# Performance work log

Measured on AMD Instinct MI355X. Metric: run time of the kernel, lower is better.

The kernel has to match this reference:

```python
import jax, jax.numpy as jnp
import numpy as np

N_NODE = 118
DM, DP, DR, DH, DN, DPHI, DE = 768, 128, 128, 256, 256, 192, 256
N_OUT = 2
NEG = -1e9

leaky = lambda z: jnp.where(z >= 0, z, 0.01 * z)


def lstm_layer(x_seq, W_ih, W_hh, b_ih, b_hh):
    # x_seq: [B, T, in]; W_ih: [4H, in]; W_hh: [4H, H]; gate order i,f,g,o (torch)
    B = x_seq.shape[0]
    H = W_hh.shape[1]

    def step(carry, xt):
        h, c = carry
        gates = xt @ W_ih.T + h @ W_hh.T + b_ih + b_hh  # [B, 4H]
        i, f, g, o = jnp.split(gates, 4, axis=1)
        c = jax.nn.sigmoid(f) * c + jax.nn.sigmoid(i) * jnp.tanh(g)
        h = jax.nn.sigmoid(o) * jnp.tanh(c)
        return (h, c), h

    h0 = jnp.zeros((B, H), x_seq.dtype)
    (_, _), hs = jax.lax.scan(step, (h0, h0), jnp.swapaxes(x_seq, 0, 1))
    return jnp.swapaxes(hs, 0, 1)  # [B, T, H]


def setup_inputs() -> dict:
    key = jax.random.key(0)
    ks = jax.random.split(key, 32)
    n_feat, T = 128, 2048
    sc = 0.05
    inp = {}
    inp["x"] = jax.random.normal(ks[0], (N_NODE, T, n_feat), jnp.float32)
    h_pmt = jax.random.uniform(ks[1], (N_NODE, 2), jnp.float32)
    act = jax.random.randint(ks[2], (N_NODE, 1), 0, 2).astype(jnp.float32)
    inp["x_tag"] = jnp.concatenate([h_pmt, act], axis=1)
    # LSTM params (2 layers, hidden=DP)
    inp["W_ih0"] = jax.random.normal(ks[3], (4 * DP, n_feat), jnp.float32) * sc
    inp["W_hh0"] = jax.random.normal(ks[4], (4 * DP, DP), jnp.float32) * sc
    inp["b_ih0"] = jnp.zeros((4 * DP,), jnp.float32)
    inp["b_hh0"] = jnp.zeros((4 * DP,), jnp.float32)
    inp["W_ih1"] = jax.random.normal(ks[5], (4 * DP, DP), jnp.float32) * sc
    inp["W_hh1"] = jax.random.normal(ks[6], (4 * DP, DP), jnp.float32) * sc
    inp["b_ih1"] = jnp.zeros((4 * DP,), jnp.float32)
    inp["b_hh1"] = jnp.zeros((4 * DP,), jnp.float32)
    inp["pseudo_message"] = jax.random.normal(ks[7], (1, DM), jnp.float32) * sc
    inp["Wum"] = jax.random.normal(ks[8], (DM + 1, DR), jnp.float32) * sc
    inp["Wvm"] = jax.random.normal(ks[9], (DM + 1, DR), jnp.float32) * sc
    inp["Wup"] = jax.random.normal(ks[10], (DP, DR), jnp.float32) * sc
    inp["Wvp"] = jax.random.normal(ks[11], (DP, DR), jnp.float32) * sc
    inp["W_hyb"] = jax.random.normal(ks[12], (3 * DR, DH), jnp.float32) * sc
    inp["b_hyb"] = jnp.zeros((DH,), jnp.float32)
    inp["W_act"] = jax.random.normal(ks[13], (DH + 2, DN), jnp.float32) * sc
    inp["b_act"] = jnp.zeros((DN,), jnp.float32)
    inp["W_inact"] = jax.random.normal(ks[14], (DH, DN), jnp.float32) * sc
    inp["b_inact"] = jnp.zeros((DN,), jnp.float32)
    inp["Wphin"] = jax.random.normal(ks[15], (2 * DN, DPHI), jnp.float32) * sc
    inp["aphi"] = jax.random.normal(ks[16], (DPHI, 1), jnp.float32) * sc
    inp["Won"] = jax.random.normal(ks[17], (2 * DN, DN), jnp.float32) * sc
    inp["Weo"] = jax.random.normal(ks[18], (3 * DN, DE), jnp.float32) * sc
    inp["Wi"] = jax.random.normal(ks[19], (N_NODE, DN + 2 * DE, N_OUT), jnp.float32) * sc
    inp["bi"] = jax.random.normal(ks[20], (N_NODE, N_OUT), jnp.float32) * sc
    return inp


def reference(x, x_tag, W_ih0, W_hh0, b_ih0, b_hh0, W_ih1, W_hh1, b_ih1, b_hh1,
              pseudo_message, Wum, Wvm, Wup, Wvp, W_hyb, b_hyb, W_act, b_act,
              W_inact, b_inact, Wphin, aphi, Won, Weo, Wi, bi):
    N = x.shape[0]
    # --- price embedding: 2-layer LSTM, take last hidden ---
    h1 = lstm_layer(x, W_ih0, W_hh0, b_ih0, b_hh0)
    h2 = lstm_layer(h1, W_ih1, W_hh1, b_ih1, b_hh1)
    p = leaky(h2[:, -1, :])  # [N, DP]

    act = x_tag[:, -1:]                      # [N, 1]
    V1 = x_tag[:, -1] == 0
    V0 = x_tag[:, -1] == 1
    m = jnp.broadcast_to(pseudo_message, (N, DM))
    v_m = leaky(jnp.concatenate([m, act], axis=1) @ Wvm)
    u_p = leaky(p @ Wup)
    h_pmt = x_tag[:, 0:2]
    h_hyb = leaky(jnp.concatenate([u_p, u_p + v_m, v_m], axis=1) @ W_hyb + b_hyb)
    n_act = (jnp.concatenate([h_hyb, h_pmt], axis=1) @ W_act + b_act) * (1.0 - act)
    n_inact = (h_hyb @ W_inact + b_inact) * act
    n = leaky(n_act + n_inact)               # [N, DN]

    # pair[i, j] = cat(n[j], n[i])  (matches unsqueeze(0)/unsqueeze(1) repeat order)
    pair = jnp.concatenate([
        jnp.broadcast_to(n[None, :, :], (N, N, DN)),
        jnp.broadcast_to(n[:, None, :], (N, N, DN)),
    ], axis=-1)                               # [N, N, 2*DN]

    phi = (leaky(pair @ Wphin) @ aphi)[..., 0]  # [N, N]
    mask1 = V1[:, None]
    mask0 = V0[:, None]
    phi1 = jax.nn.softmax(jnp.where(mask1, phi, NEG), axis=0)
    phi0 = jax.nn.softmax(jnp.where(mask0, phi, NEG), axis=0)
    phi_masked = jnp.where(mask1, phi1, jnp.where(mask0, phi0, phi))
    phi_all = jax.nn.softmax(phi, axis=0)
    alpha = jnp.where(jnp.sum(V1) > 0, phi_masked, phi_all)

    e = leaky(pair @ Won)
    e = jnp.concatenate([e, pair], axis=-1) @ Weo  # [N, N, DE]
    alpha1 = (1.0 - act) * alpha              # [N, N]
    alpha0 = act * alpha
    hyper_m1 = leaky(jnp.einsum('nj,njd->nd', alpha1, e))
    hyper_m0 = leaky(jnp.einsum('nj,njd->nd', alpha0, e))
    hyper_m = jnp.concatenate([hyper_m0, hyper_m1], axis=-1)
    output = jnp.concatenate([n, hyper_m], axis=-1)  # [N, DN+2*DE]
    y_hat = jnp.einsum('nd,ndo->no', output, Wi) + bi
    y_hat = jax.nn.softmax(y_hat, axis=1)

    o1 = Wum @ Wvm.T
    o2 = Wup @ Wvp.T
    l_ort = jnp.sqrt(jnp.sum(o1 * o1)) + jnp.sqrt(jnp.sum(o2 * o2))

    # vectorized pairwise cosine similarity * sign product over V1 nodes
    nrm = jnp.maximum(jnp.linalg.norm(n, axis=1), 1e-8)
    n_unit = n / nrm[:, None]
    s = jnp.sign(h_pmt[:, 1] - h_pmt[:, 0]) * V1.astype(n.dtype)
    l_pol = jnp.sum((n_unit @ n_unit.T) * (s[:, None] * s[None, :]))

    return (y_hat, h_pmt, l_ort, l_pol, V1, V0)
```

## Files before the change

kernel.cpp:

```cpp
#include <hip/hip_runtime.h>
#include <cstdint>
#include <cstddef>

#define NNODE 118
#define TSEQ  2048
#define TC    256
#define NCH   8
#define TGB   8
#define NEGC  -1000000000.0f

typedef __fp16 f16x8 __attribute__((ext_vector_type(8)));
typedef float floatx4 __attribute__((ext_vector_type(4)));

__device__ __forceinline__ float leakyf(float x){ return x >= 0.f ? x : 0.01f * x; }
__device__ __forceinline__ float frcp(float x){ return __builtin_amdgcn_rcpf(x); }
__device__ __forceinline__ float sigm(float x){ return frcp(1.f + __expf(-x)); }
__device__ __forceinline__ float tanhfast(float x){ return 1.f - 2.f * frcp(__expf(2.f * x) + 1.f); }

__device__ __forceinline__ int swzb(int row, int colByte){
  return row * 256 + (colByte ^ ((row & 7) << 4) ^ ((row & 8) << 2));
}

__device__ float bred_sum(float v, float* buf, int nthr){
  int tid = threadIdx.x;
  buf[tid] = v; __syncthreads();
  for (int s = nthr >> 1; s > 0; s >>= 1){
    if (tid < s) buf[tid] += buf[tid + s];
    __syncthreads();
  }
  float r = buf[0]; __syncthreads(); return r;
}
__device__ float bred_max(float v, float* buf, int nthr){
  int tid = threadIdx.x;
  buf[tid] = v; __syncthreads();
  for (int s = nthr >> 1; s > 0; s >>= 1){
    if (tid < s) buf[tid] = fmaxf(buf[tid], buf[tid + s]);
    __syncthreads();
  }
  float r = buf[0]; __syncthreads(); return r;
}

__global__ void f32_to_f16_k(const float* __restrict__ in, __fp16* __restrict__ out, int n){
  int i = blockIdx.x * blockDim.x + threadIdx.x;
  if (i < n) out[i] = (__fp16)in[i];
}

__global__ __launch_bounds__(256, 2) void gateproj(
    const float* __restrict__ x,
    const __fp16* __restrict__ ringr,
    const __fp16* __restrict__ wiA,
    const __fp16* __restrict__ wiB,
    __fp16* __restrict__ pre1o, __fp16* __restrict__ pre2o,
    int n1blocks, int t0abs)
{
  const int tid = threadIdx.x, lane = tid & 63, w4 = tid >> 6;
  const int q = lane >> 4, l16 = lane & 15;
  const bool isA = (int)blockIdx.x < n1blocks;
  const int bid = isA ? blockIdx.x : (blockIdx.x - n1blocks);
  const int tg = bid >> 3, blk = bid & 7, tbase = tg * TGB;
  const __fp16* Wf = isA ? wiA : wiB;
  __fp16* preo = isA ? pre1o : pre2o;

  __shared__ __fp16 tiles[TGB][2048];

  if (isA){
    const int node = tid >> 4, k8 = tid & 15;
    const int gnode = blk * 16 + node;
    #pragma unroll
    for (int t = 0; t < TGB; t++){
      __fp16 tmp[8];
      if (gnode < NNODE){
        const float* s = x + ((size_t)gnode * TSEQ + (t0abs + tbase + t)) * 128 + k8 * 8;
        float4 a = ((const float4*)s)[0];
        float4 b = ((const float4*)s)[1];
        tmp[0]=(__fp16)a.x; tmp[1]=(__fp16)a.y; tmp[2]=(__fp16)a.z; tmp[3]=(__fp16)a.w;
        tmp[4]=(__fp16)b.x; tmp[5]=(__fp16)b.y; tmp[6]=(__fp16)b.z; tmp[7]=(__fp16)b.w;
      } else {
        #pragma unroll
        for (int i = 0; i < 8; i++) tmp[i] = (__fp16)0.f;
      }
      *(uint4*)((char*)&tiles[t][0] + swzb(node, k8 * 16)) = *(const uint4*)tmp;
    }
  } else {
    #pragma unroll
    for (int t = 0; t < TGB; t++){
      uint4 v = *(const uint4*)((const char*)ringr + (((size_t)(tbase + t) * 8 + blk) * 4096) + tid * 16);
      *(uint4*)((char*)&tiles[t][0] + tid * 16) = v;
    }
  }

  f16x8 WB[2][4][4];
  #pragma unroll
  for (int ws = 0; ws < 2; ws++)
    #pragma unroll
    for (int g = 0; g < 4; g++){
      const int gate = g * 128 + (w4 * 2 + ws) * 16 + l16;
      const __fp16* wp = Wf + (size_t)gate * 128 + q * 8;
      #pragma unroll
      for (int kt = 0; kt < 4; kt++) WB[ws][g][kt] = *(const f16x8*)(wp + kt * 32);
    }
  __syncthreads();

  #pragma unroll 1
  for (int t = 0; t < TGB; t++){
    f16x8 ax[4];
    #pragma unroll
    for (int kt = 0; kt < 4; kt++)
      ax[kt] = *(const f16x8*)((const char*)&tiles[t][0] + swzb(l16, kt * 64 + q * 16));
    #pragma unroll
    for (int ws = 0; ws < 2; ws++){
      const size_t off = ((((size_t)(tbase + t) * 8 + blk) * 8 + (size_t)(w4 * 2 + ws)) * 64 + (size_t)lane) * 32;
      #pragma unroll
      for (int g = 0; g < 4; g++){
        floatx4 acc = {0.f, 0.f, 0.f, 0.f};
        #pragma unroll
        for (int kt = 0; kt < 4; kt++)
          acc = __builtin_amdgcn_mfma_f32_16x16x32_f16(ax[kt], WB[ws][g][kt], acc, 0, 0, 0);
        __fp16 o[4];
        o[0]=(__fp16)acc[0]; o[1]=(__fp16)acc[1]; o[2]=(__fp16)acc[2]; o[3]=(__fp16)acc[3];
        *(uint2*)((char*)preo + off + g * 8) = *(const uint2*)o;
      }
    }
  }
}

__global__ __launch_bounds__(512, 2) void lstm_scan(
    const __fp16* __restrict__ pre1, const __fp16* __restrict__ pre2,
    __fp16* __restrict__ ring,
    const __fp16* __restrict__ whh0, const __fp16* __restrict__ whh1,
    const float* __restrict__ b_ih0, const float* __restrict__ b_hh0,
    const float* __restrict__ b_ih1, const float* __restrict__ b_hh1,
    __fp16* __restrict__ hs1, float* __restrict__ c1s,
    __fp16* __restrict__ hs2, float* __restrict__ c2s,
    float* __restrict__ pout, int c)
{
  const bool isL1 = blockIdx.x < 8;
  if (isL1){ if (c >= NCH) return; } else { if (c < 1) return; }
  const int blk = blockIdx.x & 7, n0 = blk * 16;
  const int tid = threadIdx.x, lane = tid & 63, w = tid >> 6;
  const int q = lane >> 4, l16 = lane & 15;

  __shared__ __fp16 hhist[16][2048];

  const __fp16* prebase = isL1 ? pre1 : pre2;
  const __fp16* Wh = isL1 ? whh0 : whh1;
  const float* bA = isL1 ? b_ih0 : b_ih1;
  const float* bB = isL1 ? b_hh0 : b_hh1;
  __fp16* hst = isL1 ? hs1 : hs2;
  float* cst = isL1 ? c1s : c2s;
  const bool zin = isL1 ? (c == 0) : (c == 1);
  char* ringw = (char*)(ring + (size_t)(c & 1) * TC * 8 * 2048);

  f16x8 WH[4][4];
  float bias[4];
  #pragma unroll
  for (int g = 0; g < 4; g++){
    const int gate = g * 128 + w * 16 + l16;
    const __fp16* wp = Wh + (size_t)gate * 128 + q * 8;
    #pragma unroll
    for (int kt = 0; kt < 4; kt++) WH[g][kt] = *(const f16x8*)(wp + kt * 32);
    bias[g] = bA[gate] + bB[gate];
  }

  float creg[4]; __fp16 hreg[4];
  #pragma unroll
  for (int r = 0; r < 4; r++){
    const int node = q * 4 + r, d = w * 16 + l16;
    __fp16 h0;
    if (zin){ creg[r] = 0.f; h0 = (__fp16)0.f; }
    else { creg[r] = cst[(size_t)(n0 + node) * 128 + d]; h0 = hst[(size_t)(n0 + node) * 128 + d]; }
    hreg[r] = h0;
    *(__fp16*)((char*)&hhist[15][0] + swzb(node, 2 * d)) = h0;
  }

#define LDPRE(PR, T) do { \
    const char* _b = (const char*)prebase + ((((size_t)(T) * 8 + blk) * 8 + (size_t)w) * 64 + (size_t)lane) * 32; \
    PR[0] = ((const uint4*)_b)[0]; \
    PR[1] = ((const uint4*)_b)[1]; \
  } while (0)

#define STEP(P, CUR, NXT) do { \
    const char* hsrc = (const char*)&hhist[((P) + 15) & 15][0]; \
    if (isL1 && (P) >= 8 && (((P) & 7) == 0)){ \
      const int half_ = ((P) & 8) ? 0 : 8;       \
      _Pragma("unroll") \
      for (int s_ = 0; s_ < 8; s_++){ \
        uint2 hv = *(const uint2*)((const char*)&hhist[half_ + s_][0] + tid * 8); \
        *(uint2*)(ringw + (((size_t)((P) - 8 + s_) * 8 + blk) * 4096) + tid * 8) = hv; \
      } \
    } \
    floatx4 acc[4]; \
    { \
      __fp16 pva[8], pvb[8]; \
      *(uint4*)pva = CUR[0]; *(uint4*)pvb = CUR[1]; \
      _Pragma("unroll") \
      for (int i_ = 0; i_ < 4; i_++){ \
        acc[0][i_] = (float)pva[i_];     acc[1][i_] = (float)pva[4 + i_]; \
        acc[2][i_] = (float)pvb[i_];     acc[3][i_] = (float)pvb[4 + i_]; \
      } \
    } \
    if ((P) + 1 < TC) LDPRE(NXT, (P) + 1); \
    f16x8 ah[4]; \
    _Pragma("unroll") \
    for (int kt = 0; kt < 4; kt++) \
      ah[kt] = *(const f16x8*)(hsrc + swzb(l16, kt * 64 + q * 16)); \
    _Pragma("unroll") \
    for (int kt = 0; kt < 4; kt++){ \
      _Pragma("unroll") \
      for (int g = 0; g < 4; g++) \
        acc[g] = __builtin_amdgcn_mfma_f32_16x16x32_f16(ah[kt], WH[g][kt], acc[g], 0, 0, 0); \
    } \
    char* hdst = (char*)&hhist[(P) & 15][0]; \
    _Pragma("unroll") \
    for (int r = 0; r < 4; r++){ \
      const float gi = acc[0][r] + bias[0]; \
      const float gf = acc[1][r] + bias[1]; \
      const float gc = acc[2][r] + bias[2]; \
      const float go = acc[3][r] + bias[3]; \
      float cc = sigm(gf) * creg[r] + sigm(gi) * tanhfast(gc); \
      creg[r] = cc; \
      const float h = sigm(go) * tanhfast(cc); \
      hreg[r] = (__fp16)h; \
      *(__fp16*)(hdst + swzb(q * 4 + r, 2 * (w * 16 + l16))) = hreg[r]; \
    } \
    __syncthreads(); \
  } while (0)

  uint4 prA[2], prB[2];
  LDPRE(prA, 0);
  __syncthreads();

  #pragma unroll 1
  for (int p = 0; p < TC; p += 2){
    STEP(p, prA, prB);
    STEP(p + 1, prB, prA);
  }

  if (isL1){
    #pragma unroll
    for (int s_ = 0; s_ < 8; s_++){
      uint2 hv = *(const uint2*)((const char*)&hhist[8 + s_][0] + tid * 8);
      *(uint2*)(ringw + (((size_t)(TC - 8 + s_) * 8 + blk) * 4096) + tid * 8) = hv;
    }
  }
  #pragma unroll
  for (int r = 0; r < 4; r++){
    const int node = q * 4 + r, d = w * 16 + l16;
    const size_t idx = (size_t)(n0 + node) * 128 + d;
    cst[idx] = creg[r];
    hst[idx] = hreg[r];
    if (!isL1 && c == NCH && (n0 + node) < NNODE) pout[idx] = leakyf((float)hreg[r]);
  }
#undef STEP
#undef LDPRE
}

__global__ void node_mlp(
    const float* __restrict__ x_tag, const float* __restrict__ pm,
    const float* __restrict__ Wvm, const float* __restrict__ Wup,
    const float* __restrict__ W_hyb, const float* __restrict__ b_hyb,
    const float* __restrict__ W_act, const float* __restrict__ b_act,
    const float* __restrict__ W_inact, const float* __restrict__ b_inact,
    const float* __restrict__ p, float* __restrict__ nmat)
{
  int n = blockIdx.x, tid = threadIdx.x;
  __shared__ float pl[128], up[128], vm[128], hh[256];
  float act = x_tag[n * 3 + 2], hp0 = x_tag[n * 3 + 0], hp1 = x_tag[n * 3 + 1];
  if (tid < 128) pl[tid] = p[n * 128 + tid];
  __syncthreads();
  if (tid < 128){
    float a1 = 0.f;
    for (int k = 0; k < 768; k++) a1 += pm[k] * Wvm[k * 128 + tid];
    a1 += act * Wvm[768 * 128 + tid];
    vm[tid] = leakyf(a1);
    float a2 = 0.f;
    for (int k = 0; k < 128; k++) a2 += pl[k] * Wup[k * 128 + tid];
    up[tid] = leakyf(a2);
  }
  __syncthreads();
  {
    float a = b_hyb[tid];
    for (int k = 0; k < 128; k++) a += up[k] * W_hyb[k * 256 + tid];
    for (int k = 0; k < 128; k++) a += (up[k] + vm[k]) * W_hyb[(128 + k) * 256 + tid];
    for (int k = 0; k < 128; k++) a += vm[k] * W_hyb[(256 + k) * 256 + tid];
    hh[tid] = leakyf(a);
  }
  __syncthreads();
  {
    float na = b_act[tid];
    for (int k = 0; k < 256; k++) na += hh[k] * W_act[k * 256 + tid];
    na += hp0 * W_act[256 * 256 + tid] + hp1 * W_act[257 * 256 + tid];
    float ni = b_inact[tid];
    for (int k = 0; k < 256; k++) ni += hh[k] * W_inact[k * 256 + tid];
    nmat[n * 256 + tid] = leakyf(na * (1.f - act) + ni * act);
  }
}

__global__ void node_proj(
    const float* __restrict__ nmat,
    const float* __restrict__ Wphin, const float* __restrict__ Won,
    const float* __restrict__ Weo,
    float* __restrict__ A, float* __restrict__ B,
    float* __restrict__ C, float* __restrict__ D,
    float* __restrict__ Q, float* __restrict__ R)
{
  int n = blockIdx.x, tid = threadIdx.x;
  __shared__ float nl[256];
  nl[tid] = nmat[n * 256 + tid];
  __syncthreads();
  if (tid < 192){
    float a = 0.f, b = 0.f;
    for (int k = 0; k < 256; k++){ float v = nl[k]; a += v * Wphin[k * 192 + tid]; b += v * Wphin[(256 + k) * 192 + tid]; }
    A[n * 192 + tid] = a; B[n * 192 + tid] = b;
  }
  float c = 0.f, d = 0.f, q = 0.f, r = 0.f;
  for (int k = 0; k < 256; k++){
    float v = nl[k];
    c += v * Won[k * 256 + tid];
    d += v * Won[(256 + k) * 256 + tid];
    q += v * Weo[(256 + k) * 256 + tid];
    r += v * Weo[(512 + k) * 256 + tid];
  }
  C[n * 256 + tid] = c; D[n * 256 + tid] = d;
  Q[n * 256 + tid] = q; R[n * 256 + tid] = r;
}

__global__ void phi_kernel(const float* __restrict__ A, const float* __restrict__ B,
                           const float* __restrict__ aphi, float* __restrict__ phiT)
{
  int j = blockIdx.x, tid = threadIdx.x;
  __shared__ float Aj[192], ap[192];
  for (int k = tid; k < 192; k += 128){ Aj[k] = A[j * 192 + k]; ap[k] = aphi[k]; }
  __syncthreads();
  if (tid < NNODE){
    const float* Bi = B + (size_t)tid * 192;
    float s = 0.f;
    for (int k = 0; k < 192; k++) s += leakyf(Aj[k] + Bi[k]) * ap[k];
    phiT[j * NNODE + tid] = s;
  }
}

__global__ void alpha_kernel(const float* __restrict__ phiT, const float* __restrict__ x_tag,
                             float* __restrict__ alpha)
{
  int j = blockIdx.x, tid = threadIdx.x;
  __shared__ float buf[128];
  bool valid = tid < NNODE;
  float ph = valid ? phiT[j * NNODE + tid] : 0.f;
  float a  = valid ? x_tag[tid * 3 + 2] : -1.f;
  bool v1 = (a == 0.f), v0 = (a == 1.f);

  float c1 = bred_sum((valid && v1) ? 1.f : 0.f, buf, 128);

  float x1 = (valid && v1) ? ph : NEGC;
  float m1 = bred_max(valid ? x1 : -3.4e38f, buf, 128);
  float e1 = valid ? __expf(x1 - m1) : 0.f;
  float s1 = bred_sum(e1, buf, 128);
  float p1 = e1 / s1;

  float x0 = (valid && v0) ? ph : NEGC;
  float m0 = bred_max(valid ? x0 : -3.4e38f, buf, 128);
  float e0 = valid ? __expf(x0 - m0) : 0.f;
  float s0 = bred_sum(e0, buf, 128);
  float p0 = e0 / s0;

  float ma = bred_max(valid ? ph : -3.4e38f, buf, 128);
  float ea = valid ? __expf(ph - ma) : 0.f;
  float sa = bred_sum(ea, buf, 128);
  float pa = ea / sa;

  float pmask = v1 ? p1 : (v0 ? p0 : ph);
  float al = (c1 > 0.f) ? pmask : pa;
  if (valid) alpha[tid * NNODE + j] = al;
}

__global__ void att_sum(const float* __restrict__ alpha, const float* __restrict__ C,
                        const float* __restrict__ D, const float* __restrict__ Q,
                        const float* __restrict__ R, const float* __restrict__ nmat,
                        float* __restrict__ T1, float* __restrict__ Spart,
                        float* __restrict__ nrm)
{
  int i = blockIdx.x, tid = threadIdx.x;
  __shared__ float al[128];
  __shared__ float rb[256];
  if (tid < 128) al[tid] = (tid < NNODE) ? alpha[i * NNODE + tid] : 0.f;
  __syncthreads();
  float Di = D[i * 256 + tid];
  float acc1 = 0.f, acc2 = 0.f, sa = 0.f;
  for (int jj = 0; jj < NNODE; jj++){
    float av = al[jj]; sa += av;
    acc1 += av * leakyf(C[jj * 256 + tid] + Di);
    acc2 += av * Q[jj * 256 + tid];
  }
  T1[i * 256 + tid] = acc1;
  Spart[i * 256 + tid] = acc2 + sa * R[i * 256 + tid];
  float nv = nmat[i * 256 + tid];
  float ss = bred_sum(nv * nv, rb, 256);
  if (tid == 0) nrm[i] = fmaxf(sqrtf(ss), 1e-8f);
}

__global__ void finalize_node(const float* __restrict__ T1, const float* __restrict__ Spart,
                              const float* __restrict__ Weo, const float* __restrict__ nmat,
                              const float* __restrict__ x_tag, const float* __restrict__ Wi,
                              const float* __restrict__ bi, const float* __restrict__ nrm,
                              float* __restrict__ vvec, float* __restrict__ out)
{
  int i = blockIdx.x, tid = threadIdx.x;
  __shared__ float t1[256];
  __shared__ float rb[256];
  t1[tid] = T1[i * 256 + tid];
  __syncthreads();
  float s = Spart[i * 256 + tid];
  for (int k = 0; k < 256; k++) s += t1[k] * Weo[k * 256 + tid];
  float act = x_tag[i * 3 + 2], hp0 = x_tag[i * 3 + 0], hp1 = x_tag[i * 3 + 1];
  float hm0 = leakyf(act * s);
  float hm1 = leakyf((1.f - act) * s);
  float nd = nmat[i * 256 + tid];
  const float* Wir = Wi + (size_t)i * 1536;
  float y0 = nd * Wir[tid * 2]     + hm0 * Wir[(256 + tid) * 2]     + hm1 * Wir[(512 + tid) * 2];
  float y1 = nd * Wir[tid * 2 + 1] + hm0 * Wir[(256 + tid) * 2 + 1] + hm1 * Wir[(512 + tid) * 2 + 1];
  y0 = bred_sum(y0, rb, 256);
  y1 = bred_sum(y1, rb, 256);
  float sgn = (hp1 > hp0) ? 1.f : ((hp1 < hp0) ? -1.f : 0.f);
  if (act == 0.f && sgn != 0.f) atomicAdd(vvec + tid, sgn * nd / nrm[i]);
  if (tid == 0){
    y0 += bi[i * 2]; y1 += bi[i * 2 + 1];
    float m = fmaxf(y0, y1);
    float ee0 = __expf(y0 - m), ee1 = __expf(y1 - m);
    float ssum = ee0 + ee1;
    out[i * 2]     = ee0 / ssum;
    out[i * 2 + 1] = ee1 / ssum;
    out[236 + i * 2]     = hp0;
    out[236 + i * 2 + 1] = hp1;
    out[474 + i] = (act == 0.f) ? 1.f : 0.f;
    out[592 + i] = (act == 1.f) ? 1.f : 0.f;
  }
}

__global__ void ort_kernel(const float* __restrict__ Wum, const float* __restrict__ Wvm,
                           const float* __restrict__ Wup, const float* __restrict__ Wvp,
                           float* __restrict__ misc)
{
  int a = blockIdx.x, b = threadIdx.x;
  float g1 = 0.f, g2 = 0.f, g3 = 0.f, g4 = 0.f;
  for (int r = 0; r < 769; r++){
    g1 += Wum[r * 128 + a] * Wum[r * 128 + b];
    g2 += Wvm[r * 128 + a] * Wvm[r * 128 + b];
  }
  for (int r = 0; r < 128; r++){
    g3 += Wup[r * 128 + a] * Wup[r * 128 + b];
    g4 += Wvp[r * 128 + a] * Wvp[r * 128 + b];
  }
  __shared__ float rb[128];
  float s1 = bred_sum(g1 * g2, rb, 128);
  float s2 = bred_sum(g3 * g4, rb, 128);
  if (b == 0){ atomicAdd(misc + 0, s1); atomicAdd(misc + 1, s2); }
}

__global__ void finalize_scalars(const float* __restrict__ misc, const float* __restrict__ vvec,
                                 float* __restrict__ out)
{
  __shared__ float rb[256];
  int tid = threadIdx.x;
  float v = vvec[tid];
  float ss = bred_sum(v * v, rb, 256);
  if (tid == 0){
    out[472] = sqrtf(misc[0]) + sqrtf(misc[1]);
    out[473] = ss;
  }
}

extern "C" void kernel_launch(void* const* d_in, const int* in_sizes, int n_in,
                              void* d_out, int out_size, void* d_ws, size_t ws_size,
                              hipStream_t stream)
{
  const float* x        = (const float*)d_in[0];
  const float* x_tag    = (const float*)d_in[1];
  const float* W_ih0    = (const float*)d_in[2];
  const float* W_hh0    = (const float*)d_in[3];
  const float* b_ih0    = (const float*)d_in[4];
  const float* b_hh0    = (const float*)d_in[5];
  const float* W_ih1    = (const float*)d_in[6];
  const float* W_hh1    = (const float*)d_in[7];
  const float* b_ih1    = (const float*)d_in[8];
  const float* b_hh1    = (const float*)d_in[9];
  const float* pm       = (const float*)d_in[10];
  const float* Wum      = (const float*)d_in[11];
  const float* Wvm      = (const float*)d_in[12];
  const float* Wup      = (const float*)d_in[13];
  const float* Wvp      = (const float*)d_in[14];
  const float* W_hyb    = (const float*)d_in[15];
  const float* b_hyb    = (const float*)d_in[16];
  const float* W_act    = (const float*)d_in[17];
  const float* b_act    = (const float*)d_in[18];
  const float* W_inact  = (const float*)d_in[19];
  const float* b_inact  = (const float*)d_in[20];
  const float* Wphin    = (const float*)d_in[21];
  const float* aphi     = (const float*)d_in[22];
  const float* Won      = (const float*)d_in[23];
  const float* Weo      = (const float*)d_in[24];
  const float* Wi       = (const float*)d_in[25];
  const float* bi       = (const float*)d_in[26];
  float* out = (float*)d_out;

  char* base = (char*)d_ws;
  size_t off = 0;
  auto take = [&](size_t bytes) -> char* {
    char* p = base + off;
    off += (bytes + 255) & ~(size_t)255;
    return p;
  };
  __fp16* pre1   = (__fp16*)take((size_t)TC * 8 * 32 * 512);
  __fp16* pre2   = (__fp16*)take((size_t)TC * 8 * 32 * 512);
  __fp16* h1ring = (__fp16*)take((size_t)2 * TC * 8 * 2048 * 2);
  __fp16* wih0h  = (__fp16*)take((size_t)512 * 128 * 2);
  __fp16* wih1h  = (__fp16*)take((size_t)512 * 128 * 2);
  __fp16* whh0h  = (__fp16*)take((size_t)512 * 128 * 2);
  __fp16* whh1h  = (__fp16*)take((size_t)512 * 128 * 2);
  __fp16* hs1    = (__fp16*)take((size_t)128 * 128 * 2);
  float* c1s     = (float*)take((size_t)128 * 128 * 4);
  __fp16* hs2    = (__fp16*)take((size_t)128 * 128 * 2);
  float* c2s     = (float*)take((size_t)128 * 128 * 4);
  float* pbuf  = (float*)take((size_t)NNODE * 128 * 4);
  float* nmat  = (float*)take((size_t)NNODE * 256 * 4);
  float* Amat  = (float*)take((size_t)NNODE * 192 * 4);
  float* Bmat  = (float*)take((size_t)NNODE * 192 * 4);
  float* Cmat  = (float*)take((size_t)NNODE * 256 * 4);
  float* Dmat  = (float*)take((size_t)NNODE * 256 * 4);
  float* Qmat  = (float*)take((size_t)NNODE * 256 * 4);
  float* Rmat  = (float*)take((size_t)NNODE * 256 * 4);
  float* phiT  = (float*)take((size_t)NNODE * NNODE * 4);
  float* alpha = (float*)take((size_t)NNODE * NNODE * 4);
  float* T1    = (float*)take((size_t)NNODE * 256 * 4);
  float* Spart = (float*)take((size_t)NNODE * 256 * 4);
  float* nrm   = (float*)take((size_t)NNODE * 4);
  float* vvec  = (float*)take(256 * 4);
  float* misc  = (float*)take(8 * 4);

  hipMemsetAsync(vvec, 0, 1024 + 32, stream);

  f32_to_f16_k<<<256, 256, 0, stream>>>(W_ih0, wih0h, 512 * 128);
  f32_to_f16_k<<<256, 256, 0, stream>>>(W_ih1, wih1h, 512 * 128);
  f32_to_f16_k<<<256, 256, 0, stream>>>(W_hh0, whh0h, 512 * 128);
  f32_to_f16_k<<<256, 256, 0, stream>>>(W_hh1, whh1h, 512 * 128);

  const size_t ringslot = (size_t)TC * 8 * 2048;
  const int gpb = (TC / TGB) * 8;
  for (int c = 0; c <= NCH; c++){
    const int n1 = (c < NCH) ? gpb : 0;
    const int n2 = (c >= 1) ? gpb : 0;
    if (n1 + n2 > 0)
      gateproj<<<n1 + n2, 256, 0, stream>>>(x, h1ring + (size_t)((c - 1) & 1) * ringslot,
                                            wih0h, wih1h, pre1, pre2, n1, c * TC);
    lstm_scan<<<16, 512, 0, stream>>>(pre1, pre2, h1ring, whh0h, whh1h,
                                      b_ih0, b_hh0, b_ih1, b_hh1,
                                      hs1, c1s, hs2, c2s, pbuf, c);
  }

  node_mlp<<<NNODE, 256, 0, stream>>>(x_tag, pm, Wvm, Wup, W_hyb, b_hyb,
                                      W_act, b_act, W_inact, b_inact, pbuf, nmat);
  node_proj<<<NNODE, 256, 0, stream>>>(nmat, Wphin, Won, Weo, Amat, Bmat, Cmat, Dmat, Qmat, Rmat);
  phi_kernel<<<NNODE, 128, 0, stream>>>(Amat, Bmat, aphi, phiT);
  alpha_kernel<<<NNODE, 128, 0, stream>>>(phiT, x_tag, alpha);
  att_sum<<<NNODE, 256, 0, stream>>>(alpha, Cmat, Dmat, Qmat, Rmat, nmat, T1, Spart, nrm);
  finalize_node<<<NNODE, 256, 0, stream>>>(T1, Spart, Weo, nmat, x_tag, Wi, bi, nrm, vvec, out);
  ort_kernel<<<128, 128, 0, stream>>>(Wum, Wvm, Wup, Wvp, misc);
  finalize_scalars<<<1, 256, 0, stream>>>(misc, vvec, out);
}
```

Baseline: 3.350 ms.

## Fold LSTM bias into gate projection, deepen prefetch, and slim scan step barrier

Moves the bias addition out of the sequential LSTM scan into the parallel gate projection kernel, shortening the per-step critical path. The precomputed-gate prefetch now runs two steps ahead instead of one. The LSTM cell math is rewritten to share reciprocals, so one cell update uses two rcp instead of five. __syncthreads is replaced by an explicit LDS waitcnt plus s_barrier, so outstanding global loads are not waited on at each step. Adding bias before the fp16 rounding of the pre-activations slightly changes numerics, and the combined-fraction form could overflow for large gate values.

```diff
diff --git a/kernel.cpp b/kernel.cpp
--- a/kernel.cpp
+++ b/kernel.cpp
@@ -50,6 +50,8 @@
     const __fp16* __restrict__ ringr,
     const __fp16* __restrict__ wiA,
     const __fp16* __restrict__ wiB,
+    const float* __restrict__ bA_ih, const float* __restrict__ bA_hh,
+    const float* __restrict__ bB_ih, const float* __restrict__ bB_hh,
     __fp16* __restrict__ pre1o, __fp16* __restrict__ pre2o,
     int n1blocks, int t0abs)
 {
@@ -59,6 +61,8 @@
   const int bid = isA ? blockIdx.x : (blockIdx.x - n1blocks);
   const int tg = bid >> 3, blk = bid & 7, tbase = tg * TGB;
   const __fp16* Wf = isA ? wiA : wiB;
+  const float* bih = isA ? bA_ih : bB_ih;
+  const float* bhh = isA ? bA_hh : bB_hh;
   __fp16* preo = isA ? pre1o : pre2o;
 
   __shared__ __fp16 tiles[TGB][2048];
@@ -90,6 +94,7 @@
   }
 
   f16x8 WB[2][4][4];
+  float bsum[2][4];
   #pragma unroll
   for (int ws = 0; ws < 2; ws++)
     #pragma unroll
@@ -98,6 +103,7 @@
       const __fp16* wp = Wf + (size_t)gate * 128 + q * 8;
       #pragma unroll
       for (int kt = 0; kt < 4; kt++) WB[ws][g][kt] = *(const f16x8*)(wp + kt * 32);
+      bsum[ws][g] = bih[gate] + bhh[gate];
     }
   __syncthreads();
 
@@ -117,7 +123,9 @@
         for (int kt = 0; kt < 4; kt++)
           acc = __builtin_amdgcn_mfma_f32_16x16x32_f16(ax[kt], WB[ws][g][kt], acc, 0, 0, 0);
         __fp16 o[4];
-        o[0]=(__fp16)acc[0]; o[1]=(__fp16)acc[1]; o[2]=(__fp16)acc[2]; o[3]=(__fp16)acc[3];
+        const float bb = bsum[ws][g];
+        o[0]=(__fp16)(acc[0]+bb); o[1]=(__fp16)(acc[1]+bb);
+        o[2]=(__fp16)(acc[2]+bb); o[3]=(__fp16)(acc[3]+bb);
         *(uint2*)((char*)preo + off + g * 8) = *(const uint2*)o;
       }
     }
@@ -128,8 +136,6 @@
     const __fp16* __restrict__ pre1, const __fp16* __restrict__ pre2,
     __fp16* __restrict__ ring,
     const __fp16* __restrict__ whh0, const __fp16* __restrict__ whh1,
-    const float* __restrict__ b_ih0, const float* __restrict__ b_hh0,
-    const float* __restrict__ b_ih1, const float* __restrict__ b_hh1,
     __fp16* __restrict__ hs1, float* __restrict__ c1s,
     __fp16* __restrict__ hs2, float* __restrict__ c2s,
     float* __restrict__ pout, int c)
@@ -144,22 +150,18 @@
 
   const __fp16* prebase = isL1 ? pre1 : pre2;
   const __fp16* Wh = isL1 ? whh0 : whh1;
-  const float* bA = isL1 ? b_ih0 : b_ih1;
-  const float* bB = isL1 ? b_hh0 : b_hh1;
   __fp16* hst = isL1 ? hs1 : hs2;
   float* cst = isL1 ? c1s : c2s;
   const bool zin = isL1 ? (c == 0) : (c == 1);
   char* ringw = (char*)(ring + (size_t)(c & 1) * TC * 8 * 2048);
 
   f16x8 WH[4][4];
-  float bias[4];
   #pragma unroll
   for (int g = 0; g < 4; g++){
     const int gate = g * 128 + w * 16 + l16;
     const __fp16* wp = Wh + (size_t)gate * 128 + q * 8;
     #pragma unroll
     for (int kt = 0; kt < 4; kt++) WH[g][kt] = *(const f16x8*)(wp + kt * 32);
-    bias[g] = bA[gate] + bB[gate];
   }
 
   float creg[4]; __fp16 hreg[4];
@@ -179,7 +181,14 @@
     PR[1] = ((const uint4*)_b)[1]; \
   } while (0)
 
-#define STEP(P, CUR, NXT) do { \
+#define SYNC() do { \
+    __builtin_amdgcn_sched_barrier(0); \
+    asm volatile("s_waitcnt lgkmcnt(0)"); \
+    __builtin_amdgcn_sched_barrier(0); \
+    __builtin_amdgcn_s_barrier(); \
+  } while (0)
+
+#define STEP(P, CUR) do { \
     const char* hsrc = (const char*)&hhist[((P) + 15) & 15][0]; \
     if (isL1 && (P) >= 8 && (((P) & 7) == 0)){ \
       const int half_ = ((P) & 8) ? 0 : 8;       \
@@ -199,7 +208,7 @@
         acc[2][i_] = (float)pvb[i_];     acc[3][i_] = (float)pvb[4 + i_]; \
       } \
     } \
-    if ((P) + 1 < TC) LDPRE(NXT, (P) + 1); \
+    if ((P) + 2 < TC) LDPRE(CUR, (P) + 2); \
     f16x8 ah[4]; \
     _Pragma("unroll") \
     for (int kt = 0; kt < 4; kt++) \
@@ -213,27 +222,32 @@
     char* hdst = (char*)&hhist[(P) & 15][0]; \
     _Pragma("unroll") \
     for (int r = 0; r < 4; r++){ \
-      const float gi = acc[0][r] + bias[0]; \
-      const float gf = acc[1][r] + bias[1]; \
-      const float gc = acc[2][r] + bias[2]; \
-      const float go = acc[3][r] + bias[3]; \
-      float cc = sigm(gf) * creg[r] + sigm(gi) * tanhfast(gc); \
+       \
+      const float A_ = 1.f + __expf(-acc[1][r]);           \
+      const float B_ = 1.f + __expf(-acc[0][r]);           \
+      const float G_ = __expf(2.f * acc[2][r]) + 1.f;      \
+      const float BG_ = B_ * G_; \
+      const float num_ = creg[r] * BG_ + A_ * (G_ - 2.f); \
+      const float cc = num_ * frcp(A_ * BG_); \
       creg[r] = cc; \
-      const float h = sigm(go) * tanhfast(cc); \
+      const float T_ = __expf(2.f * cc) + 1.f; \
+      const float D_ = 1.f + __expf(-acc[3][r]);           \
+      const float h = (T_ - 2.f) * frcp(T_ * D_); \
       hreg[r] = (__fp16)h; \
       *(__fp16*)(hdst + swzb(q * 4 + r, 2 * (w * 16 + l16))) = hreg[r]; \
     } \
-    __syncthreads(); \
+    SYNC(); \
   } while (0)
 
   uint4 prA[2], prB[2];
   LDPRE(prA, 0);
+  LDPRE(prB, 1);
   __syncthreads();
 
   #pragma unroll 1
   for (int p = 0; p < TC; p += 2){
-    STEP(p, prA, prB);
-    STEP(p + 1, prB, prA);
+    STEP(p, prA);
+    STEP(p + 1, prB);
   }
 
   if (isL1){
@@ -252,6 +266,7 @@
     if (!isL1 && c == NCH && (n0 + node) < NNODE) pout[idx] = leakyf((float)hreg[r]);
   }
 #undef STEP
+#undef SYNC
 #undef LDPRE
 }
 
@@ -551,9 +566,10 @@
     const int n2 = (c >= 1) ? gpb : 0;
     if (n1 + n2 > 0)
       gateproj<<<n1 + n2, 256, 0, stream>>>(x, h1ring + (size_t)((c - 1) & 1) * ringslot,
-                                            wih0h, wih1h, pre1, pre2, n1, c * TC);
+                                            wih0h, wih1h,
+                                            b_ih0, b_hh0, b_ih1, b_hh1,
+                                            pre1, pre2, n1, c * TC);
     lstm_scan<<<16, 512, 0, stream>>>(pre1, pre2, h1ring, whh0h, whh1h,
-                                      b_ih0, b_hh0, b_ih1, b_hh1,
                                       hs1, c1s, hs2, c2s, pbuf, c);
   }
 
```

Result: faster. 2.953 ms (-11.8%).
